# Kernel tuning notes

Hardware: AMD Instinct MI355X
Metric: run time of the kernel (lower is better)

The kernel has to match this reference:

```python
import jax, jax.numpy as jnp
import numpy as np

N, E, T = 20000, 200000, 400000
HID, DOWN, CO, DR = 128, 32, 64, 16


def _normalize(v):
    # F.normalize(dim=-1): v / max(||v||_2, eps)
    n = jnp.linalg.norm(v, axis=-1, keepdims=True)
    return v / jnp.maximum(n, 1e-12)


def setup_inputs() -> dict:
    key = jax.random.key(0)
    ks = jax.random.split(key, 16)
    return {
        "x": jax.random.normal(ks[0], (N, HID), jnp.float32),
        "robs": jax.random.normal(ks[1], (E, DR), jnp.float32),
        "shbs": jax.random.normal(ks[2], (T, DR), jnp.float32),
        "coeffs": jax.random.normal(ks[3], (N, DR, CO), jnp.float32),
        "edge_index": jax.random.randint(ks[4], (2, E), 0, N),
        "idx_j": jax.random.randint(ks[5], (T,), 0, N),
        "idx_k": jax.random.randint(ks[6], (T,), 0, N),
        "edge_idx_kj": jax.random.randint(ks[7], (T,), 0, E),
        "edge_idx_ji": jax.random.randint(ks[8], (T,), 0, E),
        # Dense params stored as [in, out]; y = x @ W (+ b)
        "W_node1": jax.random.normal(ks[9], (HID, HID), jnp.float32) / np.sqrt(HID).astype(np.float32),
        "b_node1": jnp.zeros((HID,), jnp.float32),
        "W_node2": jax.random.normal(ks[10], (HID, DOWN), jnp.float32) / np.sqrt(HID).astype(np.float32),
        "b_node2": jnp.zeros((DOWN,), jnp.float32),
        "W_co1": jax.random.normal(ks[11], (CO, HID), jnp.float32) / np.sqrt(CO).astype(np.float32),
        "W_co2": jax.random.normal(ks[12], (HID, DOWN), jnp.float32) / np.sqrt(HID).astype(np.float32),
        "W_up": jax.random.normal(ks[13], (DOWN, HID), jnp.float32) / np.sqrt(DOWN).astype(np.float32),
    }


def reference(x, robs, shbs, coeffs, edge_index, idx_j, idx_k, edge_idx_kj,
              edge_idx_ji, W_node1, b_node1, W_node2, b_node2, W_co1, W_co2, W_up):
    silu = jax.nn.silu
    edge_src, edge_dst = edge_index[0], edge_index[1]

    # node_lin: act -> Dense(hid,hid,bias) -> act -> Dense(hid,down,bias)
    x_d = silu(silu(x) @ W_node1 + b_node1) @ W_node2 + b_node2      # [N, DOWN]

    # coeffs_lin: act -> Dense(co,hid) -> act -> Dense(hid,down), no bias
    c = silu(silu(coeffs) @ W_co1) @ W_co2                           # [N, DR, DOWN]

    # triplet interaction
    c_k = c[idx_k]                                                   # [T, DR, DOWN]
    coeffs_kj = _normalize(c_k * c[idx_j] + c_k)                     # [T, DR, DOWN]
    tw = (shbs * robs[edge_idx_kj])[..., None] * coeffs_kj           # [T, DR, DOWN]
    tw = jax.ops.segment_sum(tw, edge_idx_ji, num_segments=robs.shape[0])  # [E, DR, DOWN]

    # edge interaction
    c_d = c[edge_dst]
    coeffs_ji = _normalize((c_d * c[edge_src] + c_d) * tw)           # [E, DR, DOWN]
    r = _normalize(jnp.einsum('ed,edh->eh', robs, coeffs_ji))        # [E, DOWN]

    # aggregate to nodes and up-project
    agg = jax.ops.segment_sum(x_d[edge_dst] * r, edge_src, num_segments=x.shape[0])  # [N, DOWN]
    return agg @ W_up                                                # [N, HID]
```

## Files before the change

### kernel.cpp

```cpp
#include <hip/hip_runtime.h>
#include <hip/hip_bf16.h>

#define N_NODES 20000
#define N_EDGES 200000
#define N_TRIP  400000
#define HID 128
#define DOWN 32
#define CO 64
#define DR 16

typedef __attribute__((ext_vector_type(8))) _Float16 half8;
typedef __attribute__((ext_vector_type(4))) float f32x4;

__device__ __forceinline__ float silu_f(float v) {
    return v / (1.0f + __expf(-v));
}

__global__ void k_init(float* __restrict__ agg, int* __restrict__ head) {
    int i = blockIdx.x * blockDim.x + threadIdx.x;
    if (i < N_NODES * DOWN) agg[i] = 0.0f;
    if (i < N_EDGES) head[i] = -1;
}

__global__ void k_build(const int* __restrict__ eji, int* __restrict__ head,
                        int* __restrict__ nxt) {
    int t = blockIdx.x * blockDim.x + threadIdx.x;
    if (t < N_TRIP) {
        nxt[t] = atomicExch(&head[eji[t]], t);
    }
}

__global__ void k_prep(const float* __restrict__ Wc1, const float* __restrict__ Wc2,
                       _Float16* __restrict__ W1t, _Float16* __restrict__ W2t) {
    int i = blockIdx.x * blockDim.x + threadIdx.x;
    if (i < HID * CO)   W1t[i] = (_Float16)Wc1[(i & (CO - 1)) * HID + (i >> 6)];
    if (i < DOWN * HID) W2t[i] = (_Float16)Wc2[(i & (HID - 1)) * DOWN + (i >> 7)];
}

__global__ __launch_bounds__(256) void k_node(
    const float* __restrict__ x, const float* __restrict__ W1,
    const float* __restrict__ b1, const float* __restrict__ W2,
    const float* __restrict__ b2, float* __restrict__ x_d) {
    __shared__ float sx[4][4][HID];
    __shared__ float sh[4][4][HID];
    const int wave = threadIdx.x >> 6, lane = threadIdx.x & 63;
    const int row0 = (blockIdx.x * 4 + wave) * 4;

    #pragma unroll
    for (int r = 0; r < 4; ++r) {
        sx[wave][r][lane]      = silu_f(x[(row0 + r) * HID + lane]);
        sx[wave][r][lane + 64] = silu_f(x[(row0 + r) * HID + lane + 64]);
    }
    __syncthreads();

    float acc[4][2] = {};
    for (int k = 0; k < HID; ++k) {
        float wa = W1[k * HID + lane];
        float wb = W1[k * HID + lane + 64];
        #pragma unroll
        for (int r = 0; r < 4; ++r) {
            float s = sx[wave][r][k];
            acc[r][0] = fmaf(s, wa, acc[r][0]);
            acc[r][1] = fmaf(s, wb, acc[r][1]);
        }
    }
    float ba = b1[lane], bb = b1[lane + 64];
    #pragma unroll
    for (int r = 0; r < 4; ++r) {
        sh[wave][r][lane]      = silu_f(acc[r][0] + ba);
        sh[wave][r][lane + 64] = silu_f(acc[r][1] + bb);
    }
    __syncthreads();

    const int m = lane & 31, kh = lane >> 5;
    float a2[4] = {};
    for (int kk = 0; kk < 64; ++kk) {
        int k = kh * 64 + kk;
        float w = W2[k * DOWN + m];
        #pragma unroll
        for (int r = 0; r < 4; ++r) a2[r] = fmaf(sh[wave][r][k], w, a2[r]);
    }
    #pragma unroll
    for (int r = 0; r < 4; ++r) a2[r] += __shfl_xor(a2[r], 32);
    if (kh == 0) {
        float bm = b2[m];
        #pragma unroll
        for (int r = 0; r < 4; ++r) x_d[(row0 + r) * DOWN + m] = a2[r] + bm;
    }
}

__global__ __launch_bounds__(256) void k_co(
    const float* __restrict__ cf, const _Float16* __restrict__ W1t,
    const _Float16* __restrict__ W2t, _Float16* __restrict__ ch) {
    __shared__ __align__(16) _Float16 sh[4][16 * 136];
    const int wave = threadIdx.x >> 6, lane = threadIdx.x & 63;
    const int m = lane & 15, q = lane >> 4;
    const int row0 = blockIdx.x * 64 + wave * 16;

    const float* ar = cf + (row0 + m) * CO + q * 8;
    half8 aA, aB;
    #pragma unroll
    for (int j = 0; j < 8; ++j) aA[j] = (_Float16)silu_f(ar[j]);
    #pragma unroll
    for (int j = 0; j < 8; ++j) aB[j] = (_Float16)silu_f(ar[32 + j]);

    const half8* b1p = (const half8*)W1t;
    f32x4 acc[8];
    #pragma unroll
    for (int nt = 0; nt < 8; ++nt) {
        f32x4 z = {0.0f, 0.0f, 0.0f, 0.0f};
        half8 b0 = b1p[(nt * 16 + m) * 8 + q];
        half8 b1 = b1p[(nt * 16 + m) * 8 + 4 + q];
        z       = __builtin_amdgcn_mfma_f32_16x16x32_f16(aA, b0, z, 0, 0, 0);
        acc[nt] = __builtin_amdgcn_mfma_f32_16x16x32_f16(aB, b1, z, 0, 0, 0);
    }

    _Float16* shw = sh[wave];
    #pragma unroll
    for (int nt = 0; nt < 8; ++nt) {
        #pragma unroll
        for (int r = 0; r < 4; ++r)
            shw[(q * 4 + r) * 136 + nt * 16 + m] = (_Float16)silu_f(acc[nt][r]);
    }

    const half8* b2p = (const half8*)W2t;
    f32x4 c0 = {0.0f, 0.0f, 0.0f, 0.0f}, c1 = {0.0f, 0.0f, 0.0f, 0.0f};
    #pragma unroll
    for (int ks = 0; ks < 4; ++ks) {
        half8 a = *(const half8*)(shw + m * 136 + ks * 32 + q * 8);
        half8 bb0 = b2p[m * 16 + ks * 4 + q];
        half8 bb1 = b2p[(16 + m) * 16 + ks * 4 + q];
        c0 = __builtin_amdgcn_mfma_f32_16x16x32_f16(a, bb0, c0, 0, 0, 0);
        c1 = __builtin_amdgcn_mfma_f32_16x16x32_f16(a, bb1, c1, 0, 0, 0);
    }
    #pragma unroll
    for (int r = 0; r < 4; ++r) {
        int rg = (row0 + q * 4 + r) * DOWN;
        ch[rg + m]      = (_Float16)c0[r];
        ch[rg + 16 + m] = (_Float16)c1[r];
    }
}

__global__ __launch_bounds__(256) void k_edge(
    const _Float16* __restrict__ ch, const float* __restrict__ x_d,
    const float* __restrict__ robs, const float* __restrict__ shbs,
    const int* __restrict__ esrc, const int* __restrict__ edst,
    const int* __restrict__ idxj, const int* __restrict__ idxk,
    const int* __restrict__ ekj, const int* __restrict__ head,
    const int* __restrict__ nxt, float* __restrict__ agg) {
    __shared__ float rbuf[4][DOWN];
    const int wave = threadIdx.x >> 6, lane = threadIdx.x & 63;
    const int e = blockIdx.x * 4 + wave;
    const int dr = lane >> 2, q = lane & 3;
    const half8* cp = (const half8*)ch;

    const int en_s = esrc[e], en_d = edst[e];
    half8 hd = cp[en_d * 64 + lane];
    half8 hs = cp[en_s * 64 + lane];
    float rob = robs[e * DR + dr];
    float xd = (lane < DOWN) ? x_d[en_d * DOWN + lane] : 0.0f;

    float tw[8];
    #pragma unroll
    for (int j = 0; j < 8; ++j) tw[j] = 0.0f;

    int t = head[e];
    while (t >= 0) {
        const int tn = nxt[t];
        const int nk = idxk[t], nj = idxj[t], kj = ekj[t];
        const float sw = shbs[t * DR + dr];
        half8 hk = cp[nk * 64 + lane];
        half8 hj = cp[nj * 64 + lane];
        const float rb = robs[kj * DR + dr];
        float u[8];
        float ss = 0.0f;
        #pragma unroll
        for (int j = 0; j < 8; ++j) {
            float ckj = (float)hk[j], cjj = (float)hj[j];
            u[j] = fmaf(ckj, cjj, ckj);
            ss = fmaf(u[j], u[j], ss);
        }
        ss += __shfl_xor(ss, 1);
        ss += __shfl_xor(ss, 2);
        float w = sw * rb * __frsqrt_rn(fmaxf(ss, 1e-24f));
        #pragma unroll
        for (int j = 0; j < 8; ++j) tw[j] = fmaf(w, u[j], tw[j]);
        t = tn;
    }

    float v[8];
    float ss2 = 0.0f;
    #pragma unroll
    for (int j = 0; j < 8; ++j) {
        float cdj = (float)hd[j], csj = (float)hs[j];
        v[j] = fmaf(cdj, csj, cdj) * tw[j];
        ss2 = fmaf(v[j], v[j], ss2);
    }
    ss2 += __shfl_xor(ss2, 1);
    ss2 += __shfl_xor(ss2, 2);
    float inv2 = __frsqrt_rn(fmaxf(ss2, 1e-24f));

    float rj[8];
    #pragma unroll
    for (int j = 0; j < 8; ++j) rj[j] = v[j] * inv2 * rob;
    #pragma unroll
    for (int j = 0; j < 8; ++j) {
        rj[j] += __shfl_xor(rj[j], 4);
        rj[j] += __shfl_xor(rj[j], 8);
        rj[j] += __shfl_xor(rj[j], 16);
        rj[j] += __shfl_xor(rj[j], 32);
    }
    float s3 = 0.0f;
    #pragma unroll
    for (int j = 0; j < 8; ++j) s3 = fmaf(rj[j], rj[j], s3);
    s3 += __shfl_xor(s3, 1);
    s3 += __shfl_xor(s3, 2);
    float inv3 = __frsqrt_rn(fmaxf(s3, 1e-24f));

    if (lane < 4) {
        #pragma unroll
        for (int j = 0; j < 8; ++j) rbuf[wave][q * 8 + j] = rj[j] * inv3;
    }
    if (lane < DOWN) {
        atomicAdd(&agg[en_s * DOWN + lane], xd * rbuf[wave][lane]);
    }
}

__global__ __launch_bounds__(256) void k_up(
    const float* __restrict__ agg, const float* __restrict__ Wup,
    float* __restrict__ out) {
    const int wave = threadIdx.x >> 6, lane = threadIdx.x & 63;
    const int row0 = (blockIdx.x * 4 + wave) * 4;
    float acc[4][2] = {};
    for (int k = 0; k < DOWN; ++k) {
        float wa = Wup[k * HID + lane];
        float wb = Wup[k * HID + lane + 64];
        #pragma unroll
        for (int r = 0; r < 4; ++r) {
            float a = agg[(row0 + r) * DOWN + k];
            acc[r][0] = fmaf(a, wa, acc[r][0]);
            acc[r][1] = fmaf(a, wb, acc[r][1]);
        }
    }
    #pragma unroll
    for (int r = 0; r < 4; ++r) {
        out[(row0 + r) * HID + lane]      = acc[r][0];
        out[(row0 + r) * HID + lane + 64] = acc[r][1];
    }
}

extern "C" void kernel_launch(void* const* d_in, const int* in_sizes, int n_in,
                              void* d_out, int out_size, void* d_ws, size_t ws_size,
                              hipStream_t stream) {
    const float* x    = (const float*)d_in[0];
    const float* robs = (const float*)d_in[1];
    const float* shbs = (const float*)d_in[2];
    const float* cf   = (const float*)d_in[3];
    const int*   eidx = (const int*)d_in[4];
    const int*   idxj = (const int*)d_in[5];
    const int*   idxk = (const int*)d_in[6];
    const int*   ekj  = (const int*)d_in[7];
    const int*   eji  = (const int*)d_in[8];
    const float* W1   = (const float*)d_in[9];
    const float* b1   = (const float*)d_in[10];
    const float* W2   = (const float*)d_in[11];
    const float* b2   = (const float*)d_in[12];
    const float* Wc1  = (const float*)d_in[13];
    const float* Wc2  = (const float*)d_in[14];
    const float* Wup  = (const float*)d_in[15];
    const int* esrc = eidx;
    const int* edst = eidx + N_EDGES;
    float* out = (float*)d_out;

    float*    x_d  = (float*)d_ws;
    float*    agg  = x_d + (size_t)N_NODES * DOWN;
    int*      head = (int*)(agg + (size_t)N_NODES * DOWN);
    int*      nxt  = head + N_EDGES;
    _Float16* ch   = (_Float16*)(nxt + N_TRIP);
    _Float16* W1t  = ch + (size_t)N_NODES * DR * DOWN;
    _Float16* W2t  = W1t + HID * CO;

    k_init <<<(N_NODES * DOWN + 255) / 256, 256, 0, stream>>>(agg, head);
    k_build<<<(N_TRIP + 255) / 256, 256, 0, stream>>>(eji, head, nxt);
    k_prep <<<(HID * CO + 255) / 256, 256, 0, stream>>>(Wc1, Wc2, W1t, W2t);
    k_node <<<N_NODES / 16, 256, 0, stream>>>(x, W1, b1, W2, b2, x_d);
    k_co   <<<(N_NODES * DR) / 64, 256, 0, stream>>>(cf, W1t, W2t, ch);
    k_edge <<<N_EDGES / 4, 256, 0, stream>>>(ch, x_d, robs, shbs, esrc, edst,
                                             idxj, idxk, ekj, head, nxt, agg);
    k_up   <<<N_NODES / 16, 256, 0, stream>>>(agg, Wup, out);
}
```

Baseline: 457.1 us.

## Fuse setup and node/coeff MLP kernels, prefetch next triplet in edge loop

Merges the init and weight-prep kernels into one setup kernel, and merges the node MLP and coefficient MLP into one launch that branches on block index, so fewer kernels are launched and the two independent MLPs can run side by side. The edge kernel's linked-list walk now loads the next triplet's gathered coefficients and scalars while the current one is being computed, to hide gather latency. The coefficient loads switch to float4 vector reads. The costs are higher register pressure in the edge loop and one extra block of shared memory per block in the fused kernel.

```diff
diff --git a/kernel.cpp b/kernel.cpp
--- a/kernel.cpp
+++ b/kernel.cpp
@@ -9,6 +9,9 @@
 #define CO 64
 #define DR 16
 
+#define NODE_BLOCKS 1250
+#define CO_BLOCKS   5000
+
 typedef __attribute__((ext_vector_type(8))) _Float16 half8;
 typedef __attribute__((ext_vector_type(4))) float f32x4;
 
@@ -16,10 +19,14 @@
     return v / (1.0f + __expf(-v));
 }
 
-__global__ void k_init(float* __restrict__ agg, int* __restrict__ head) {
+__global__ void k_setup(float* __restrict__ agg, int* __restrict__ head,
+                        const float* __restrict__ Wc1, const float* __restrict__ Wc2,
+                        _Float16* __restrict__ W1t, _Float16* __restrict__ W2t) {
     int i = blockIdx.x * blockDim.x + threadIdx.x;
     if (i < N_NODES * DOWN) agg[i] = 0.0f;
     if (i < N_EDGES) head[i] = -1;
+    if (i < HID * CO)   W1t[i] = (_Float16)Wc1[(i & (CO - 1)) * HID + (i >> 6)];
+    if (i < DOWN * HID) W2t[i] = (_Float16)Wc2[(i & (HID - 1)) * DOWN + (i >> 7)];
 }
 
 __global__ void k_build(const int* __restrict__ eji, int* __restrict__ head,
@@ -30,114 +37,115 @@
     }
 }
 
-__global__ void k_prep(const float* __restrict__ Wc1, const float* __restrict__ Wc2,
-                       _Float16* __restrict__ W1t, _Float16* __restrict__ W2t) {
-    int i = blockIdx.x * blockDim.x + threadIdx.x;
-    if (i < HID * CO)   W1t[i] = (_Float16)Wc1[(i & (CO - 1)) * HID + (i >> 6)];
-    if (i < DOWN * HID) W2t[i] = (_Float16)Wc2[(i & (HID - 1)) * DOWN + (i >> 7)];
-}
-
-__global__ __launch_bounds__(256) void k_node(
+__global__ __launch_bounds__(256) void k_nodeco(
     const float* __restrict__ x, const float* __restrict__ W1,
     const float* __restrict__ b1, const float* __restrict__ W2,
-    const float* __restrict__ b2, float* __restrict__ x_d) {
-    __shared__ float sx[4][4][HID];
-    __shared__ float sh[4][4][HID];
-    const int wave = threadIdx.x >> 6, lane = threadIdx.x & 63;
-    const int row0 = (blockIdx.x * 4 + wave) * 4;
-
-    #pragma unroll
-    for (int r = 0; r < 4; ++r) {
-        sx[wave][r][lane]      = silu_f(x[(row0 + r) * HID + lane]);
-        sx[wave][r][lane + 64] = silu_f(x[(row0 + r) * HID + lane + 64]);
-    }
-    __syncthreads();
-
-    float acc[4][2] = {};
-    for (int k = 0; k < HID; ++k) {
-        float wa = W1[k * HID + lane];
-        float wb = W1[k * HID + lane + 64];
-        #pragma unroll
-        for (int r = 0; r < 4; ++r) {
-            float s = sx[wave][r][k];
-            acc[r][0] = fmaf(s, wa, acc[r][0]);
-            acc[r][1] = fmaf(s, wb, acc[r][1]);
-        }
-    }
-    float ba = b1[lane], bb = b1[lane + 64];
-    #pragma unroll
-    for (int r = 0; r < 4; ++r) {
-        sh[wave][r][lane]      = silu_f(acc[r][0] + ba);
-        sh[wave][r][lane + 64] = silu_f(acc[r][1] + bb);
-    }
-    __syncthreads();
-
-    const int m = lane & 31, kh = lane >> 5;
-    float a2[4] = {};
-    for (int kk = 0; kk < 64; ++kk) {
-        int k = kh * 64 + kk;
-        float w = W2[k * DOWN + m];
-        #pragma unroll
-        for (int r = 0; r < 4; ++r) a2[r] = fmaf(sh[wave][r][k], w, a2[r]);
-    }
-    #pragma unroll
-    for (int r = 0; r < 4; ++r) a2[r] += __shfl_xor(a2[r], 32);
-    if (kh == 0) {
-        float bm = b2[m];
-        #pragma unroll
-        for (int r = 0; r < 4; ++r) x_d[(row0 + r) * DOWN + m] = a2[r] + bm;
-    }
-}
-
-__global__ __launch_bounds__(256) void k_co(
+    const float* __restrict__ b2, float* __restrict__ x_d,
     const float* __restrict__ cf, const _Float16* __restrict__ W1t,
     const _Float16* __restrict__ W2t, _Float16* __restrict__ ch) {
-    __shared__ __align__(16) _Float16 sh[4][16 * 136];
+    __shared__ __align__(16) char smem[4 * 16 * 136 * 2];
     const int wave = threadIdx.x >> 6, lane = threadIdx.x & 63;
-    const int m = lane & 15, q = lane >> 4;
-    const int row0 = blockIdx.x * 64 + wave * 16;
-
-    const float* ar = cf + (row0 + m) * CO + q * 8;
-    half8 aA, aB;
-    #pragma unroll
-    for (int j = 0; j < 8; ++j) aA[j] = (_Float16)silu_f(ar[j]);
-    #pragma unroll
-    for (int j = 0; j < 8; ++j) aB[j] = (_Float16)silu_f(ar[32 + j]);
-
-    const half8* b1p = (const half8*)W1t;
-    f32x4 acc[8];
-    #pragma unroll
-    for (int nt = 0; nt < 8; ++nt) {
-        f32x4 z = {0.0f, 0.0f, 0.0f, 0.0f};
-        half8 b0 = b1p[(nt * 16 + m) * 8 + q];
-        half8 b1 = b1p[(nt * 16 + m) * 8 + 4 + q];
-        z       = __builtin_amdgcn_mfma_f32_16x16x32_f16(aA, b0, z, 0, 0, 0);
-        acc[nt] = __builtin_amdgcn_mfma_f32_16x16x32_f16(aB, b1, z, 0, 0, 0);
-    }
-
-    _Float16* shw = sh[wave];
-    #pragma unroll
-    for (int nt = 0; nt < 8; ++nt) {
-        #pragma unroll
-        for (int r = 0; r < 4; ++r)
-            shw[(q * 4 + r) * 136 + nt * 16 + m] = (_Float16)silu_f(acc[nt][r]);
-    }
-
-    const half8* b2p = (const half8*)W2t;
-    f32x4 c0 = {0.0f, 0.0f, 0.0f, 0.0f}, c1 = {0.0f, 0.0f, 0.0f, 0.0f};
-    #pragma unroll
-    for (int ks = 0; ks < 4; ++ks) {
-        half8 a = *(const half8*)(shw + m * 136 + ks * 32 + q * 8);
-        half8 bb0 = b2p[m * 16 + ks * 4 + q];
-        half8 bb1 = b2p[(16 + m) * 16 + ks * 4 + q];
-        c0 = __builtin_amdgcn_mfma_f32_16x16x32_f16(a, bb0, c0, 0, 0, 0);
-        c1 = __builtin_amdgcn_mfma_f32_16x16x32_f16(a, bb1, c1, 0, 0, 0);
-    }
-    #pragma unroll
-    for (int r = 0; r < 4; ++r) {
-        int rg = (row0 + q * 4 + r) * DOWN;
-        ch[rg + m]      = (_Float16)c0[r];
-        ch[rg + 16 + m] = (_Float16)c1[r];
+
+    if (blockIdx.x < NODE_BLOCKS) {
+        float (*sx)[4][HID] = (float (*)[4][HID])smem;
+        float (*sh)[4][HID] = (float (*)[4][HID])(smem + 8192);
+        const int row0 = (blockIdx.x * 4 + wave) * 4;
+
+        #pragma unroll
+        for (int r = 0; r < 4; ++r) {
+            sx[wave][r][lane]      = silu_f(x[(row0 + r) * HID + lane]);
+            sx[wave][r][lane + 64] = silu_f(x[(row0 + r) * HID + lane + 64]);
+        }
+        __syncthreads();
+
+        float acc[4][2] = {};
+        for (int k = 0; k < HID; ++k) {
+            float wa = W1[k * HID + lane];
+            float wb = W1[k * HID + lane + 64];
+            #pragma unroll
+            for (int r = 0; r < 4; ++r) {
+                float s = sx[wave][r][k];
+                acc[r][0] = fmaf(s, wa, acc[r][0]);
+                acc[r][1] = fmaf(s, wb, acc[r][1]);
+            }
+        }
+        float ba = b1[lane], bb = b1[lane + 64];
+        #pragma unroll
+        for (int r = 0; r < 4; ++r) {
+            sh[wave][r][lane]      = silu_f(acc[r][0] + ba);
+            sh[wave][r][lane + 64] = silu_f(acc[r][1] + bb);
+        }
+        __syncthreads();
+
+        const int m = lane & 31, kh = lane >> 5;
+        float a2[4] = {};
+        for (int kk = 0; kk < 64; ++kk) {
+            int k = kh * 64 + kk;
+            float w = W2[k * DOWN + m];
+            #pragma unroll
+            for (int r = 0; r < 4; ++r) a2[r] = fmaf(sh[wave][r][k], w, a2[r]);
+        }
+        #pragma unroll
+        for (int r = 0; r < 4; ++r) a2[r] += __shfl_xor(a2[r], 32);
+        if (kh == 0) {
+            float bm = b2[m];
+            #pragma unroll
+            for (int r = 0; r < 4; ++r) x_d[(row0 + r) * DOWN + m] = a2[r] + bm;
+        }
+    } else {
+        _Float16 (*sh)[16 * 136] = (_Float16 (*)[16 * 136])smem;
+        const int m = lane & 15, q = lane >> 4;
+        const int row0 = (blockIdx.x - NODE_BLOCKS) * 64 + wave * 16;
+
+        const float* ar = cf + (row0 + m) * CO + q * 8;
+        f32x4 a0 = ((const f32x4*)ar)[0];
+        f32x4 a1 = ((const f32x4*)ar)[1];
+        f32x4 a2v = ((const f32x4*)(ar + 32))[0];
+        f32x4 a3v = ((const f32x4*)(ar + 32))[1];
+        half8 aA, aB;
+        #pragma unroll
+        for (int j = 0; j < 4; ++j) {
+            aA[j]     = (_Float16)silu_f(a0[j]);
+            aA[j + 4] = (_Float16)silu_f(a1[j]);
+            aB[j]     = (_Float16)silu_f(a2v[j]);
+            aB[j + 4] = (_Float16)silu_f(a3v[j]);
+        }
+
+        const half8* b1p = (const half8*)W1t;
+        f32x4 acc[8];
+        #pragma unroll
+        for (int nt = 0; nt < 8; ++nt) {
+            f32x4 z = {0.0f, 0.0f, 0.0f, 0.0f};
+            half8 b0 = b1p[(nt * 16 + m) * 8 + q];
+            half8 b1h = b1p[(nt * 16 + m) * 8 + 4 + q];
+            z       = __builtin_amdgcn_mfma_f32_16x16x32_f16(aA, b0, z, 0, 0, 0);
+            acc[nt] = __builtin_amdgcn_mfma_f32_16x16x32_f16(aB, b1h, z, 0, 0, 0);
+        }
+
+        _Float16* shw = sh[wave];
+        #pragma unroll
+        for (int nt = 0; nt < 8; ++nt) {
+            #pragma unroll
+            for (int r = 0; r < 4; ++r)
+                shw[(q * 4 + r) * 136 + nt * 16 + m] = (_Float16)silu_f(acc[nt][r]);
+        }
+
+        const half8* b2p = (const half8*)W2t;
+        f32x4 c0 = {0.0f, 0.0f, 0.0f, 0.0f}, c1 = {0.0f, 0.0f, 0.0f, 0.0f};
+        #pragma unroll
+        for (int ks = 0; ks < 4; ++ks) {
+            half8 a = *(const half8*)(shw + m * 136 + ks * 32 + q * 8);
+            half8 bb0 = b2p[m * 16 + ks * 4 + q];
+            half8 bb1 = b2p[(16 + m) * 16 + ks * 4 + q];
+            c0 = __builtin_amdgcn_mfma_f32_16x16x32_f16(a, bb0, c0, 0, 0, 0);
+            c1 = __builtin_amdgcn_mfma_f32_16x16x32_f16(a, bb1, c1, 0, 0, 0);
+        }
+        #pragma unroll
+        for (int r = 0; r < 4; ++r) {
+            int rg = (row0 + q * 4 + r) * DOWN;
+            ch[rg + m]      = (_Float16)c0[r];
+            ch[rg + 16 + m] = (_Float16)c1[r];
+        }
     }
 }
 
@@ -165,13 +173,26 @@
     for (int j = 0; j < 8; ++j) tw[j] = 0.0f;
 
     int t = head[e];
+    half8 hk, hj;
+    float sw, rb;
+    if (t >= 0) {
+        int nk = idxk[t], nj = idxj[t], kj = ekj[t];
+        hk = cp[nk * 64 + lane];
+        hj = cp[nj * 64 + lane];
+        sw = shbs[t * DR + dr];
+        rb = robs[kj * DR + dr];
+    }
     while (t >= 0) {
         const int tn = nxt[t];
-        const int nk = idxk[t], nj = idxj[t], kj = ekj[t];
-        const float sw = shbs[t * DR + dr];
-        half8 hk = cp[nk * 64 + lane];
-        half8 hj = cp[nj * 64 + lane];
-        const float rb = robs[kj * DR + dr];
+        half8 hk2, hj2;
+        float sw2, rb2;
+        if (tn >= 0) {
+            int nk = idxk[tn], nj = idxj[tn], kj = ekj[tn];
+            hk2 = cp[nk * 64 + lane];
+            hj2 = cp[nj * 64 + lane];
+            sw2 = shbs[tn * DR + dr];
+            rb2 = robs[kj * DR + dr];
+        }
         float u[8];
         float ss = 0.0f;
         #pragma unroll
@@ -185,6 +206,7 @@
         float w = sw * rb * __frsqrt_rn(fmaxf(ss, 1e-24f));
         #pragma unroll
         for (int j = 0; j < 8; ++j) tw[j] = fmaf(w, u[j], tw[j]);
+        hk = hk2; hj = hj2; sw = sw2; rb = rb2;
         t = tn;
     }
 
@@ -280,12 +302,11 @@
     _Float16* W1t  = ch + (size_t)N_NODES * DR * DOWN;
     _Float16* W2t  = W1t + HID * CO;
 
-    k_init <<<(N_NODES * DOWN + 255) / 256, 256, 0, stream>>>(agg, head);
-    k_build<<<(N_TRIP + 255) / 256, 256, 0, stream>>>(eji, head, nxt);
-    k_prep <<<(HID * CO + 255) / 256, 256, 0, stream>>>(Wc1, Wc2, W1t, W2t);
-    k_node <<<N_NODES / 16, 256, 0, stream>>>(x, W1, b1, W2, b2, x_d);
-    k_co   <<<(N_NODES * DR) / 64, 256, 0, stream>>>(cf, W1t, W2t, ch);
-    k_edge <<<N_EDGES / 4, 256, 0, stream>>>(ch, x_d, robs, shbs, esrc, edst,
-                                             idxj, idxk, ekj, head, nxt, agg);
-    k_up   <<<N_NODES / 16, 256, 0, stream>>>(agg, Wup, out);
-}
+    k_setup <<<(N_NODES * DOWN + 255) / 256, 256, 0, stream>>>(agg, head, Wc1, Wc2, W1t, W2t);
+    k_build <<<(N_TRIP + 255) / 256, 256, 0, stream>>>(eji, head, nxt);
+    k_nodeco<<<NODE_BLOCKS + CO_BLOCKS, 256, 0, stream>>>(x, W1, b1, W2, b2, x_d,
+                                                          cf, W1t, W2t, ch);
+    k_edge  <<<N_EDGES / 4, 256, 0, stream>>>(ch, x_d, robs, shbs, esrc, edst,
+                                              idxj, idxk, ekj, head, nxt, agg);
+    k_up    <<<N_NODES / 16, 256, 0, stream>>>(agg, Wup, out);
+}
```

After: 454.5 us. No clear change (-0.6%).
